# Optimization experiments

Hardware: AMD Instinct MI355X
Metric: run time of the kernel (lower is better)

Reference implementation:

```python
import jax, jax.numpy as jnp
import numpy as np

H = 12      # num_heads
EPS = 1e-5  # LayerNorm eps (torch default)


def _ln(x, g, b):
    m = x.mean(-1, keepdims=True)
    v = x.var(-1, keepdims=True)
    return (x - m) * jax.lax.rsqrt(v + EPS) * g + b


def _rot_half(x):
    x1, x2 = x[..., 0::2], x[..., 1::2]
    return jnp.stack((-x2, x1), axis=-1).reshape(x.shape)


def _rope_tables(n, head_dim):
    # rotary-embedding-torch: RotaryEmbedding(dim=head_dim//2, use_xpos=True),
    # theta=10000, scale_base=512. Only first rot=head_dim//2 dims are rotated.
    rot = head_dim // 2
    inv = 1.0 / (10000.0 ** (jnp.arange(0, rot, 2, dtype=jnp.float32) / rot))
    t = jnp.arange(n, dtype=jnp.float32)
    freqs = jnp.repeat(t[:, None] * inv[None, :], 2, axis=-1)  # (n, rot), interleaved
    base = (jnp.arange(0, rot, 2, dtype=jnp.float32) + 0.4 * rot) / (1.4 * rot)
    power = (t - n // 2) / 512.0
    sc = base[None, :] ** power[:, None]
    sc = jnp.concatenate([sc, sc], axis=-1)  # (n, rot), concatenated (library behavior)
    return jnp.cos(freqs), jnp.sin(freqs), sc


def _attn_path(xn, Wqkv, bqkv, Wproj, bproj, qg, qb, kg, kb, R, rg, rb):
    B, N, D = xn.shape
    d = D // H
    qkv = xn @ Wqkv + bqkv
    q, k, v = jnp.split(qkv, 3, axis=-1)
    hd = lambda t: t.reshape(B, N, H, d).transpose(0, 2, 1, 3)  # (B,H,N,d)
    q, k, v = hd(q), hd(k), hd(v)
    q = _ln(q, qg, qb)  # per-head QK LayerNorm
    k = _ln(k, kg, kb)
    cos, sin, sc = _rope_tables(N, d)
    rot = d // 2

    def rope(t, s):  # rotate only first rot dims
        tl, tr = t[..., :rot], t[..., rot:]
        tl = tl * cos * s + _rot_half(tl) * sin * s
        return jnp.concatenate([tl, tr], axis=-1)

    q = rope(q, sc)
    v = rope(v, 1.0 / sc)  # source applies rope to (q, v), not k

    scores = jnp.einsum('bhid,bhjd->bhij', q, k) / jnp.sqrt(jnp.asarray(d, xn.dtype))
    p = jax.nn.softmax(scores, axis=-1)
    # SDPA(q,k,ones_NN)[...,i,j] == sum_k p[...,i,k] for every j (constant over j).
    # All downstream ops (head-mix einsum, LayerNorm over heads, @ v) therefore
    # reduce exactly to the per-(b,i) computation below, avoiding an N^3 matmul.
    s = p.sum(-1)                              # (B,H,N)
    mix = jnp.einsum('bhi,hg->big', s, R)      # (B,N,H)
    w = _ln(mix, rg, rb)                       # reattn LayerNorm over head axis
    vsum = v.sum(axis=2)                       # (B,H,d); (w @ v) with w const over j
    y = jnp.einsum('big,bgd->bigd', w, vsum).reshape(B, N, D)
    return y @ Wproj + bproj


def _cgmlp(xn, W1, b1, gg, gb, cw, cb, W2, b2):
    h = jax.nn.gelu(xn @ W1 + b1, approximate=False)
    c2 = h.shape[-1] // 2
    xr, xg = h[..., :c2], h[..., c2:]
    xg = _ln(xg, gg, gb).transpose(0, 2, 1)  # (B,C,T)
    K = cw.shape[-1]
    xg = jax.lax.conv_general_dilated(xg, cw, (1,), [((K - 1) // 2, (K - 1) // 2)],
                                      dimension_numbers=('NCH', 'OIH', 'NCH'),
                                      feature_group_count=c2)  # depthwise conv1d
    xg = (xg + cb[None, :, None]).transpose(0, 2, 1)
    return (xr * xg) @ W2 + b2


def reference(x, Wqkv, bqkv, Wproj, bproj, qn_g, qn_b, kn_g, kn_b, reattn_w, rn_g, rn_b,
              ln1_g, ln1_b, ln2_g, ln2_b, ls1, ls2, W1, b1, gn_g, gn_b, conv_w, conv_b,
              W2, b2, Wout, bout):
    # eval mode: dropout / drop_path are identity
    xa = _ln(x, ln1_g, ln1_b)
    attn = sum(_attn_path(xa, Wqkv[p], bqkv[p], Wproj[p], bproj[p], qn_g[p], qn_b[p],
                          kn_g[p], kn_b[p], reattn_w[p], rn_g[p], rn_b[p])
               for p in range(2))
    x_attn = x + ls1 * attn
    xm = _ln(x, ln2_g, ln2_b)
    x_mlp = x + ls2 * _cgmlp(xm, W1, b1, gn_g, gn_b, conv_w, conv_b, W2, b2)
    xf = jnp.concatenate([x_attn, x_mlp], axis=-1)
    return xf @ Wout + bout + x


def setup_inputs():
    B, N, D, P = 4, 1024, 768, 2
    d = D // H
    C = 4 * D
    c2 = C // 2
    K = 21
    ks = iter(jax.random.split(jax.random.key(0), 16))
    nrm = lambda s, sd=0.02: jax.random.normal(next(ks), s, jnp.float32) * sd
    return {
        'x': jax.random.normal(next(ks), (B, N, D), jnp.float32),
        'Wqkv': nrm((P, D, 3 * D)), 'bqkv': jnp.zeros((P, 3 * D)),
        'Wproj': nrm((P, D, D)), 'bproj': jnp.zeros((P, D)),
        'qn_g': jnp.ones((P, d)), 'qn_b': jnp.zeros((P, d)),
        'kn_g': jnp.ones((P, d)), 'kn_b': jnp.zeros((P, d)),
        'reattn_w': jax.random.normal(next(ks), (P, H, H), jnp.float32),
        'rn_g': jnp.ones((P, H)), 'rn_b': jnp.zeros((P, H)),
        'ln1_g': jnp.ones((D,)), 'ln1_b': jnp.zeros((D,)),
        'ln2_g': jnp.ones((D,)), 'ln2_b': jnp.zeros((D,)),
        'ls1': jnp.full((D,), 0.01, jnp.float32), 'ls2': jnp.full((D,), 0.01, jnp.float32),
        'W1': nrm((D, C)), 'b1': jnp.zeros((C,)),
        'gn_g': jnp.ones((c2,)), 'gn_b': jnp.zeros((c2,)),
        'conv_w': nrm((c2, 1, K), 0.1), 'conv_b': jnp.zeros((c2,)),
        'W2': nrm((c2, D)), 'b2': jnp.zeros((D,)),
        'Wout': nrm((2 * D, D)), 'bout': jnp.zeros((D,)),
    }
```

## Files before the change

### kernel.cpp

```cpp
#include <hip/hip_runtime.h>
#include <hip/hip_bf16.h>

typedef short s16x8 __attribute__((ext_vector_type(8)));
typedef float f32x4 __attribute__((ext_vector_type(4)));

#define C2 1536

__device__ __forceinline__ float b2f(ushort u){ return __uint_as_float(((unsigned)u)<<16); }
__device__ __forceinline__ ushort f2b(float f){ unsigned u = __float_as_uint(f); return (ushort)((u + 0x7fffu + ((u>>16)&1u)) >> 16); }

template<int EPI, int BM, int BN>
__global__ __launch_bounds__(256) void gemm_bf16(
    const ushort* __restrict__ A, const ushort* __restrict__ BT,
    int M, int N, int K,
    const float* __restrict__ bias, const float* __restrict__ scale,
    const float* __restrict__ xres,
    ushort* __restrict__ o16, ushort* __restrict__ o16b, float* __restrict__ o32)
{
    constexpr int CA = BM*4, CB = BN*4;
    constexpr int WM = BM/2, WN = BN/2;
    constexpr int MT = WM/16, NT = WN/16;
    __shared__ ushort Al[BM*32];
    __shared__ ushort Bl[BN*32];
    const int t = threadIdx.x;
    const int m0 = blockIdx.y*BM, n0 = blockIdx.x*BN;
    const int lane = t & 63, wv = t >> 6;
    const int wm = (wv>>1)*WM, wn = (wv&1)*WN;
    const int r0 = lane & 15, q = lane >> 4;

    const int cA0 = t, cA1 = t + 256;
    const int cB0 = t, cB1 = t + 256;
    const int rA0 = ((cA0>>6)<<4)|(cA0&15), kA0 = ((cA0>>4)&3)<<3;
    const int rA1 = ((cA1>>6)<<4)|(cA1&15), kA1 = ((cA1>>4)&3)<<3;
    const int rB0 = ((cB0>>6)<<4)|(cB0&15), kB0 = ((cB0>>4)&3)<<3;
    const int rB1 = ((cB1>>6)<<4)|(cB1&15), kB1 = ((cB1>>4)&3)<<3;
    const ushort* gA0 = A  + (size_t)(m0+rA0)*K + kA0;
    const ushort* gB0 = BT + (size_t)(n0+rB0)*K + kB0;
    const ushort* gA1 = A  + (size_t)(m0+(CA>256?rA1:0))*K + kA1;
    const ushort* gB1 = BT + (size_t)(n0+(CB>256?rB1:0))*K + kB1;

    f32x4 acc[MT][NT];
    #pragma unroll
    for (int i=0;i<MT;++i)
        #pragma unroll
        for (int j=0;j<NT;++j) acc[i][j] = (f32x4){0.f,0.f,0.f,0.f};

    const int nkt = K >> 5;
    uint4 ra0, rb0, ra1, rb1;
    ra0 = *(const uint4*)gA0;
    rb0 = *(const uint4*)gB0;
    if constexpr (CA > 256) ra1 = *(const uint4*)gA1;
    if constexpr (CB > 256) rb1 = *(const uint4*)gB1;

    for (int kt = 0; kt < nkt; ++kt) {
        __syncthreads();
        *(uint4*)&Al[cA0*8] = ra0;
        *(uint4*)&Bl[cB0*8] = rb0;
        if constexpr (CA > 256) *(uint4*)&Al[cA1*8] = ra1;
        if constexpr (CB > 256) *(uint4*)&Bl[cB1*8] = rb1;
        __syncthreads();
        if (kt+1 < nkt) {
            ra0 = *(const uint4*)(gA0 + (kt+1)*32);
            rb0 = *(const uint4*)(gB0 + (kt+1)*32);
            if constexpr (CA > 256) ra1 = *(const uint4*)(gA1 + (kt+1)*32);
            if constexpr (CB > 256) rb1 = *(const uint4*)(gB1 + (kt+1)*32);
        }
        s16x8 af[MT], bfr[NT];
        #pragma unroll
        for (int mt=0; mt<MT; ++mt) af[mt]  = *(const s16x8*)&Al[(((wm>>4)+mt)*64 + lane)*8];
        #pragma unroll
        for (int nt=0; nt<NT; ++nt) bfr[nt] = *(const s16x8*)&Bl[(((wn>>4)+nt)*64 + lane)*8];
        #pragma unroll
        for (int mt=0; mt<MT; ++mt)
            #pragma unroll
            for (int nt=0; nt<NT; ++nt)
                acc[mt][nt] = __builtin_amdgcn_mfma_f32_16x16x32_bf16(af[mt], bfr[nt], acc[mt][nt], 0,0,0);
    }

    #pragma unroll
    for (int mt=0; mt<MT; ++mt) {
        #pragma unroll
        for (int nt=0; nt<NT; ++nt) {
            int col = n0 + wn + nt*16 + r0;
            #pragma unroll
            for (int r=0; r<4; ++r) {
                int row = m0 + wm + mt*16 + q*4 + r;
                float v = acc[mt][nt][r];
                if (EPI == 0) {
                    o16[(size_t)row*N + col] = f2b(v + bias[col]);
                } else if (EPI == 1) {
                    v += bias[col];
                    float g = 0.5f*v*(1.0f + erff(v*0.70710678118f));
                    if (col < C2) o16 [(size_t)row*C2 + col]        = f2b(g);
                    else          o16b[(size_t)row*C2 + (col - C2)] = f2b(g);
                } else if (EPI == 2) {
                    v += bias[col];
                    o16[(size_t)row*1536 + 768 + col] = f2b(xres[(size_t)row*768 + col] + scale[col]*v);
                } else {
                    o32[(size_t)row*768 + col] = v + bias[col] + xres[(size_t)row*768 + col];
                }
            }
        }
    }
}

__global__ __launch_bounds__(256) void pack_bt(const float* __restrict__ src, ushort* __restrict__ dst,
                                               int K, int ld, int coff)
{
    __shared__ float tl[32*33];
    int kt = blockIdx.x*32, nt = blockIdx.y*32;
    int nl = threadIdx.x & 31, kg = threadIdx.x >> 5;
    #pragma unroll
    for (int kk=0; kk<4; ++kk) {
        int k = kg*4 + kk;
        tl[k*33 + nl] = src[(size_t)(kt + k)*ld + coff + nt + nl];
    }
    __syncthreads();
    int kcol = threadIdx.x & 31, ng = threadIdx.x >> 5;
    #pragma unroll
    for (int nn=0; nn<4; ++nn) {
        int nrow = ng*4 + nn;
        dst[(size_t)(nt + nrow)*K + kt + kcol] = f2b(tl[kcol*33 + nrow]);
    }
}

__global__ __launch_bounds__(256) void pack_bv(const float* __restrict__ bqkv, float* __restrict__ bvp)
{
    int idx = blockIdx.x*256 + threadIdx.x;
    if (idx < 1536) bvp[idx] = bqkv[(idx/768)*2304 + 1536 + (idx%768)];
}

__global__ __launch_bounds__(256) void ln_x_kernel(const float* __restrict__ x,
    const float* __restrict__ g1, const float* __restrict__ b1,
    const float* __restrict__ g2, const float* __restrict__ b2,
    ushort* __restrict__ xa, ushort* __restrict__ xm)
{
    __shared__ float sb[8];
    int row = blockIdx.x; int t = threadIdx.x;
    float v[3]; float s = 0.f, ss = 0.f;
    #pragma unroll
    for (int e=0; e<3; ++e) { v[e] = x[(size_t)row*768 + t + e*256]; s += v[e]; ss += v[e]*v[e]; }
    for (int o=32; o>0; o>>=1){ s += __shfl_down(s,o,64); ss += __shfl_down(ss,o,64); }
    int lane = t&63, w = t>>6;
    if (lane==0){ sb[w]=s; sb[4+w]=ss; }
    __syncthreads();
    s = sb[0]+sb[1]+sb[2]+sb[3]; ss = sb[4]+sb[5]+sb[6]+sb[7];
    float mean = s*(1.f/768.f);
    float var  = ss*(1.f/768.f) - mean*mean;
    float rstd = rsqrtf(var + 1e-5f);
    #pragma unroll
    for (int e=0; e<3; ++e){
        int c = t + e*256;
        float n = (v[e]-mean)*rstd;
        xa[(size_t)row*768 + c] = f2b(n*g1[c] + b1[c]);
        xm[(size_t)row*768 + c] = f2b(n*g2[c] + b2[c]);
    }
}

__global__ __launch_bounds__(256) void prep_kernel(
    float* __restrict__ w1t, float* __restrict__ w2t, float* __restrict__ wvec,
    float* __restrict__ attn_c, float* __restrict__ vsum,
    const float* __restrict__ R, const float* __restrict__ rng,
    const float* __restrict__ rnb, const float* __restrict__ bproj)
{
    int idx = blockIdx.x*256 + threadIdx.x;
    {
        int i = idx >> 6, j = idx & 63;
        float w1, w2;
        if (j < 32) {
            int m = j >> 1;
            float inv = powf(10000.f, -(float)m*(1.f/16.f));
            float fr = (float)i * inv;
            float c = cosf(fr), sn = sinf(fr);
            float power = ((float)i - 512.f) * (1.f/512.f);
            float basev = (2.f*(float)(j & 15) + 12.8f) * (1.f/44.8f);
            float sfac = powf(basev, -power);
            w1 = c * sfac;
            w2 = ((j & 1) ? sn : -sn) * sfac;
        } else { w1 = 1.f; w2 = 0.f; }
        w1t[idx] = w1; w2t[idx] = w2;
    }
    if (blockIdx.x >= 1 && blockIdx.x <= 12) {
        int k = (blockIdx.x-1)*256 + threadIdx.x;
        int o = k % 768;
        attn_c[k] = bproj[o] + bproj[768 + o];
    }
    if (blockIdx.x >= 13 && blockIdx.x <= 36) {
        int k = (blockIdx.x-13)*256 + threadIdx.x;
        vsum[k] = 0.f;
    }
    if (blockIdx.x == 0) {
        __shared__ float mixs[24];
        __shared__ float ws[24];
        int t = threadIdx.x;
        if (t < 24) {
            int p = t / 12, g = t % 12;
            float m = 0.f;
            for (int h=0; h<12; ++h) m += R[p*144 + h*12 + g];
            mixs[t] = m;
        }
        __syncthreads();
        if (t < 2) {
            float mean=0.f, var=0.f;
            for (int g=0; g<12; ++g) mean += mixs[t*12+g];
            mean *= (1.f/12.f);
            for (int g=0; g<12; ++g){ float d = mixs[t*12+g]-mean; var += d*d; }
            var *= (1.f/12.f);
            float rstd = rsqrtf(var + 1e-5f);
            for (int g=0; g<12; ++g)
                ws[t*12+g] = (mixs[t*12+g]-mean)*rstd*rng[t*12+g] + rnb[t*12+g];
        }
        __syncthreads();
        if (t < 24) wvec[t] = ws[t];
    }
}

__global__ __launch_bounds__(256) void rope_reduce(const ushort* __restrict__ V,
    const float* __restrict__ w1t, const float* __restrict__ w2t, float* __restrict__ vsum)
{
    int col = blockIdx.x*256 + threadIdx.x;
    int b = blockIdx.y;
    int i0 = blockIdx.z * 256;
    int j = col & 63;
    float acc = 0.f;
    const ushort* vp = V + (size_t)(b*1024 + i0)*1536;
    #pragma unroll 4
    for (int i=0; i<256; ++i) {
        float v1 = b2f(vp[(size_t)i*1536 + col]);
        float v2 = b2f(vp[(size_t)i*1536 + (col^1)]);
        int ii = i0 + i;
        acc += w1t[ii*64 + j]*v1 + w2t[ii*64 + j]*v2;
    }
    atomicAdd(&vsum[b*1536 + col], acc);
}

__global__ __launch_bounds__(256) void attn_gemm(const float* __restrict__ vsum,
    const float* __restrict__ wvec, const float* __restrict__ Wproj, float* __restrict__ attn_c)
{
    int o  = blockIdx.x*256 + threadIdx.x;
    int c0 = blockIdx.y * 96;
    int b  = blockIdx.z;
    int p  = c0 / 768;
    float acc = 0.f;
    #pragma unroll 4
    for (int cc=0; cc<96; ++cc) {
        int c = c0 + cc;
        int cl = c - p*768;
        float y = wvec[p*12 + (cl>>6)] * vsum[b*1536 + c];
        acc += y * Wproj[(size_t)p*589824 + (size_t)cl*768 + o];
    }
    atomicAdd(&attn_c[b*768 + o], acc);
}

__global__ __launch_bounds__(256) void xf_left(const float* __restrict__ x, const float* __restrict__ ls1,
    const float* __restrict__ attn_c, ushort* __restrict__ xf)
{
    int col = blockIdx.x*256 + threadIdx.x;
    int row = blockIdx.y;
    xf[(size_t)row*1536 + col] = f2b(x[(size_t)row*768 + col] + ls1[col]*attn_c[(row>>10)*768 + col]);
}

__global__ __launch_bounds__(256) void ln_gate(const ushort* __restrict__ xg,
    const float* __restrict__ g, const float* __restrict__ bta, ushort* __restrict__ out)
{
    __shared__ float sb[8];
    int row = blockIdx.x, t = threadIdx.x;
    float v[6]; float s=0.f, ss=0.f;
    #pragma unroll
    for (int e=0;e<6;++e){ v[e] = b2f(xg[(size_t)row*1536 + t + e*256]); s+=v[e]; ss+=v[e]*v[e]; }
    for (int o=32; o>0; o>>=1){ s += __shfl_down(s,o,64); ss += __shfl_down(ss,o,64); }
    int lane = t&63, w = t>>6;
    if (lane==0){ sb[w]=s; sb[4+w]=ss; }
    __syncthreads();
    s = sb[0]+sb[1]+sb[2]+sb[3]; ss = sb[4]+sb[5]+sb[6]+sb[7];
    float mean = s*(1.f/1536.f);
    float var  = ss*(1.f/1536.f) - mean*mean;
    float rstd = rsqrtf(var + 1e-5f);
    #pragma unroll
    for (int e=0;e<6;++e){
        int c = t + e*256;
        out[(size_t)row*1536 + c] = f2b((v[e]-mean)*rstd*g[c] + bta[c]);
    }
}

#define CROWS 128
#define CIN   (CROWS + 20)
#define CSTR  72
__global__ __launch_bounds__(256) void conv_mul(const ushort* __restrict__ xgln,
    const float* __restrict__ cw, const float* __restrict__ cb,
    const ushort* __restrict__ xr, ushort* __restrict__ u)
{
    __shared__ ushort tile[CIN * CSTR];
    const int c0 = blockIdx.x * 64;
    const int i0 = blockIdx.y * CROWS;
    const int b  = blockIdx.z;
    const int t  = threadIdx.x;
    const size_t base = (size_t)b*1024*1536;

    #pragma unroll
    for (int it = 0; it < 5; ++it) {
        int idx = it*256 + t;
        if (idx < CIN*8) {
            int r  = idx >> 3;
            int cq = (idx & 7) * 8;
            int si = i0 + r - 10;
            uint4 val = make_uint4(0u,0u,0u,0u);
            if (si >= 0 && si < 1024)
                val = *(const uint4*)(xgln + base + (size_t)si*1536 + c0 + cq);
            *(uint4*)&tile[r*CSTR + cq] = val;
        }
    }
    __syncthreads();

    const int ch = t & 63;
    const int o0 = (t >> 6) * 32;
    const int c  = c0 + ch;

    float w[21];
    #pragma unroll
    for (int k=0; k<21; ++k) w[k] = cw[c*21 + k];
    const float bias = cb[c];

    float win[21];
    #pragma unroll
    for (int j=0; j<20; ++j) win[j] = b2f(tile[(o0+j)*CSTR + ch]);

    #pragma unroll
    for (int j=0; j<32; ++j) {
        win[(j+20)%21] = b2f(tile[(o0+j+20)*CSTR + ch]);
        float acc = bias;
        #pragma unroll
        for (int k=0; k<21; ++k) acc += win[(j+k)%21] * w[k];
        size_t off = base + (size_t)(i0+o0+j)*1536 + c;
        u[off] = f2b(b2f(xr[off]) * acc);
    }
}

extern "C" void kernel_launch(void* const* d_in, const int* in_sizes, int n_in,
                              void* d_out, int out_size, void* d_ws, size_t ws_size,
                              hipStream_t stream)
{
    const float* x     = (const float*)d_in[0];
    const float* Wqkv  = (const float*)d_in[1];
    const float* bqkv  = (const float*)d_in[2];
    const float* Wproj = (const float*)d_in[3];
    const float* bproj = (const float*)d_in[4];
    const float* Rw    = (const float*)d_in[9];
    const float* rng   = (const float*)d_in[10];
    const float* rnb   = (const float*)d_in[11];
    const float* ln1g  = (const float*)d_in[12];
    const float* ln1b  = (const float*)d_in[13];
    const float* ln2g  = (const float*)d_in[14];
    const float* ln2b  = (const float*)d_in[15];
    const float* ls1   = (const float*)d_in[16];
    const float* ls2   = (const float*)d_in[17];
    const float* W1    = (const float*)d_in[18];
    const float* b1    = (const float*)d_in[19];
    const float* gng   = (const float*)d_in[20];
    const float* gnb   = (const float*)d_in[21];
    const float* cw    = (const float*)d_in[22];
    const float* cb    = (const float*)d_in[23];
    const float* W2    = (const float*)d_in[24];
    const float* b2    = (const float*)d_in[25];
    const float* Wout  = (const float*)d_in[26];
    const float* bout  = (const float*)d_in[27];
    float* out = (float*)d_out;

    char* ws = (char*)d_ws;
    size_t off = 0;
    auto alloc = [&](size_t bytes)->char* {
        char* p = ws + off;
        off += (bytes + 255) & ~(size_t)255;
        return p;
    };
    ushort* WvT   = (ushort*)alloc(1536*768*2);
    ushort* W1T   = (ushort*)alloc(3072*768*2);
    ushort* W2T   = (ushort*)alloc(768*1536*2);
    ushort* WoutT = (ushort*)alloc(768*1536*2);
    float*  bvp   = (float*)alloc(1536*4);
    float*  w1t   = (float*)alloc(65536*4);
    float*  w2t   = (float*)alloc(65536*4);
    float*  wvec  = (float*)alloc(24*4);
    float*  attnc = (float*)alloc(3072*4);
    float*  vsum  = (float*)alloc(6144*4);
    ushort* xa16  = (ushort*)alloc(4096*768*2);
    ushort* xm16  = (ushort*)alloc(4096*768*2);
    ushort* V16   = (ushort*)alloc(4096*1536*2);
    ushort* xg16  = (ushort*)alloc(4096*1536*2);
    ushort* xf16  = (ushort*)alloc(4096*1536*2);
    ushort* xgln  = xa16;
    ushort* xr16  = V16;
    ushort* u16   = xg16;
    (void)ws_size; (void)n_in; (void)in_sizes; (void)out_size;

    for (int p = 0; p < 2; ++p)
        pack_bt<<<dim3(24, 24), 256, 0, stream>>>(Wqkv + (size_t)p*768*2304, WvT + (size_t)p*768*768,
                                                  768, 2304, 1536);
    pack_bt<<<dim3(24, 96), 256, 0, stream>>>(W1,   W1T,   768,  3072, 0);
    pack_bt<<<dim3(48, 24), 256, 0, stream>>>(W2,   W2T,   1536, 768,  0);
    pack_bt<<<dim3(48, 24), 256, 0, stream>>>(Wout, WoutT, 1536, 768,  0);
    pack_bv<<<dim3(6), 256, 0, stream>>>(bqkv, bvp);
    prep_kernel<<<dim3(256), 256, 0, stream>>>(w1t, w2t, wvec, attnc, vsum, Rw, rng, rnb, bproj);

    ln_x_kernel<<<dim3(4096), 256, 0, stream>>>(x, ln1g, ln1b, ln2g, ln2b, xa16, xm16);

    gemm_bf16<0,64,128><<<dim3(12, 64), 256, 0, stream>>>(xa16, WvT, 4096, 1536, 768,
                                                   bvp, nullptr, nullptr, V16, nullptr, nullptr);
    rope_reduce<<<dim3(6, 4, 4), 256, 0, stream>>>(V16, w1t, w2t, vsum);
    attn_gemm<<<dim3(3, 16, 4), 256, 0, stream>>>(vsum, wvec, Wproj, attnc);
    xf_left<<<dim3(3, 4096), 256, 0, stream>>>(x, ls1, attnc, xf16);

    gemm_bf16<1,128,128><<<dim3(24, 32), 256, 0, stream>>>(xm16, W1T, 4096, 3072, 768,
                                                   b1, nullptr, nullptr, xr16, xg16, nullptr);
    ln_gate<<<dim3(4096), 256, 0, stream>>>(xg16, gng, gnb, xgln);
    conv_mul<<<dim3(24, 8, 4), 256, 0, stream>>>(xgln, cw, cb, xr16, u16);
    gemm_bf16<2,64,64><<<dim3(12, 64), 256, 0, stream>>>(u16, W2T, 4096, 768, 1536,
                                                  b2, ls2, x, xf16, nullptr, nullptr);
    gemm_bf16<3,64,64><<<dim3(12, 64), 256, 0, stream>>>(xf16, WoutT, 4096, 768, 1536,
                                                  bout, nullptr, x, nullptr, nullptr, out);
}
```

Measured before the change: 385.2 us.

## Fold W2 into Wout and reassociate V rope-reduction to skip V GEMM

The code precomputes a combined weight (ls2-scaled Wout lower half times W2, plus the summed Wout halves) so the W2 GEMM and the Wout GEMM merge into one K=2304 GEMM over [x | u]. Constant terms (attention output, biases) are folded into a per-batch bias vector cvec. The full 4096x1536 V projection GEMM plus rope reduction becomes a small transpose, GEMMs of xa^T against the rope tables, and a contraction with WvT, so the large V intermediate is never built. This cuts FLOPs and memory traffic but adds several small serial kernels and extra weight prep per call. It also changes rounding, since x is rounded to bf16 and the W2·Wout product is precomputed in bf16.

```diff
diff --git a/kernel.cpp b/kernel.cpp
--- a/kernel.cpp
+++ b/kernel.cpp
@@ -12,9 +12,8 @@
 template<int EPI, int BM, int BN>
 __global__ __launch_bounds__(256) void gemm_bf16(
     const ushort* __restrict__ A, const ushort* __restrict__ BT,
-    int M, int N, int K,
-    const float* __restrict__ bias, const float* __restrict__ scale,
-    const float* __restrict__ xres,
+    int M, int N, int K, int lda,
+    const float* __restrict__ bias, const float* __restrict__ xres,
     ushort* __restrict__ o16, ushort* __restrict__ o16b, float* __restrict__ o32)
 {
     constexpr int CA = BM*4, CB = BN*4;
@@ -29,15 +28,12 @@
     const int r0 = lane & 15, q = lane >> 4;
 
     const int cA0 = t, cA1 = t + 256;
-    const int cB0 = t, cB1 = t + 256;
     const int rA0 = ((cA0>>6)<<4)|(cA0&15), kA0 = ((cA0>>4)&3)<<3;
     const int rA1 = ((cA1>>6)<<4)|(cA1&15), kA1 = ((cA1>>4)&3)<<3;
-    const int rB0 = ((cB0>>6)<<4)|(cB0&15), kB0 = ((cB0>>4)&3)<<3;
-    const int rB1 = ((cB1>>6)<<4)|(cB1&15), kB1 = ((cB1>>4)&3)<<3;
-    const ushort* gA0 = A  + (size_t)(m0+rA0)*K + kA0;
-    const ushort* gB0 = BT + (size_t)(n0+rB0)*K + kB0;
-    const ushort* gA1 = A  + (size_t)(m0+(CA>256?rA1:0))*K + kA1;
-    const ushort* gB1 = BT + (size_t)(n0+(CB>256?rB1:0))*K + kB1;
+    const ushort* gA0 = A  + (size_t)(m0+rA0)*lda + kA0;
+    const ushort* gB0 = BT + (size_t)(n0+rA0)*K   + kA0;
+    const ushort* gA1 = A  + (size_t)(m0+(CA>256?rA1:0))*lda + kA1;
+    const ushort* gB1 = BT + (size_t)(n0+(CB>256?rA1:0))*K   + kA1;
 
     f32x4 acc[MT][NT];
     #pragma unroll
@@ -55,9 +51,9 @@
     for (int kt = 0; kt < nkt; ++kt) {
         __syncthreads();
         *(uint4*)&Al[cA0*8] = ra0;
-        *(uint4*)&Bl[cB0*8] = rb0;
+        *(uint4*)&Bl[cA0*8] = rb0;
         if constexpr (CA > 256) *(uint4*)&Al[cA1*8] = ra1;
-        if constexpr (CB > 256) *(uint4*)&Bl[cB1*8] = rb1;
+        if constexpr (CB > 256) *(uint4*)&Bl[cA1*8] = rb1;
         __syncthreads();
         if (kt+1 < nkt) {
             ra0 = *(const uint4*)(gA0 + (kt+1)*32);
@@ -86,18 +82,17 @@
             for (int r=0; r<4; ++r) {
                 int row = m0 + wm + mt*16 + q*4 + r;
                 float v = acc[mt][nt][r];
-                if (EPI == 0) {
-                    o16[(size_t)row*N + col] = f2b(v + bias[col]);
-                } else if (EPI == 1) {
+                if (EPI == 1) {
                     v += bias[col];
                     float g = 0.5f*v*(1.0f + erff(v*0.70710678118f));
                     if (col < C2) o16 [(size_t)row*C2 + col]        = f2b(g);
                     else          o16b[(size_t)row*C2 + (col - C2)] = f2b(g);
-                } else if (EPI == 2) {
-                    v += bias[col];
-                    o16[(size_t)row*1536 + 768 + col] = f2b(xres[(size_t)row*768 + col] + scale[col]*v);
-                } else {
-                    o32[(size_t)row*768 + col] = v + bias[col] + xres[(size_t)row*768 + col];
+                } else if (EPI == 3) {
+                    o32[(size_t)row*768 + col] = v + bias[(row>>10)*768 + col] + xres[(size_t)row*768 + col];
+                } else if (EPI == 4) {
+                    o16[(size_t)row*2304 + 768 + col] = f2b(v);
+                } else if (EPI == 5) {
+                    o32[(size_t)row*N + col] = v;
                 }
             }
         }
@@ -105,7 +100,7 @@
 }
 
 __global__ __launch_bounds__(256) void pack_bt(const float* __restrict__ src, ushort* __restrict__ dst,
-                                               int K, int ld, int coff)
+                                               int K, int ld, int coff, const float* __restrict__ scale)
 {
     __shared__ float tl[32*33];
     int kt = blockIdx.x*32, nt = blockIdx.y*32;
@@ -120,8 +115,53 @@
     #pragma unroll
     for (int nn=0; nn<4; ++nn) {
         int nrow = ng*4 + nn;
-        dst[(size_t)(nt + nrow)*K + kt + kcol] = f2b(tl[kcol*33 + nrow]);
-    }
+        float s = scale ? scale[kt + kcol] : 1.0f;
+        dst[(size_t)(nt + nrow)*K + kt + kcol] = f2b(tl[kcol*33 + nrow] * s);
+    }
+}
+
+__global__ __launch_bounds__(256) void pack_wsum(const float* __restrict__ Wout, ushort* __restrict__ dst)
+{
+    __shared__ float tl[32*33];
+    int kt = blockIdx.x*32, nt = blockIdx.y*32;
+    int nl = threadIdx.x & 31, kg = threadIdx.x >> 5;
+    #pragma unroll
+    for (int kk=0; kk<4; ++kk) {
+        int k = kg*4 + kk;
+        tl[k*33 + nl] = Wout[(size_t)(kt + k)*768 + nt + nl] + Wout[(size_t)(768 + kt + k)*768 + nt + nl];
+    }
+    __syncthreads();
+    int kcol = threadIdx.x & 31, ng = threadIdx.x >> 5;
+    #pragma unroll
+    for (int nn=0; nn<4; ++nn) {
+        int nrow = ng*4 + nn;
+        dst[(size_t)(nt + nrow)*2304 + kt + kcol] = f2b(tl[kcol*33 + nrow]);
+    }
+}
+
+__global__ __launch_bounds__(256) void tr_bf16(const ushort* __restrict__ src, ushort* __restrict__ dst)
+{
+    __shared__ ushort tl[32*33];
+    int rt = blockIdx.x*32, ct = blockIdx.y*32;
+    int cl = threadIdx.x & 31, rg = threadIdx.x >> 5;
+    #pragma unroll
+    for (int rr=0; rr<4; ++rr) {
+        int r = rg*4 + rr;
+        tl[r*33 + cl] = src[(size_t)(rt + r)*768 + ct + cl];
+    }
+    __syncthreads();
+    int rcol = threadIdx.x & 31, cg = threadIdx.x >> 5;
+    #pragma unroll
+    for (int cc=0; cc<4; ++cc) {
+        int crow = cg*4 + cc;
+        dst[(size_t)(ct + crow)*4096 + rt + rcol] = tl[rcol*33 + crow];
+    }
+}
+
+__global__ __launch_bounds__(256) void pack_cast(const float* __restrict__ src, ushort* __restrict__ dst)
+{
+    int idx = blockIdx.x*256 + threadIdx.x;
+    dst[idx] = f2b(src[idx]);
 }
 
 __global__ __launch_bounds__(256) void pack_bv(const float* __restrict__ bqkv, float* __restrict__ bvp)
@@ -133,7 +173,7 @@
 __global__ __launch_bounds__(256) void ln_x_kernel(const float* __restrict__ x,
     const float* __restrict__ g1, const float* __restrict__ b1,
     const float* __restrict__ g2, const float* __restrict__ b2,
-    ushort* __restrict__ xa, ushort* __restrict__ xm)
+    ushort* __restrict__ xa, ushort* __restrict__ xm, ushort* __restrict__ xb)
 {
     __shared__ float sb[8];
     int row = blockIdx.x; int t = threadIdx.x;
@@ -154,14 +194,15 @@
         float n = (v[e]-mean)*rstd;
         xa[(size_t)row*768 + c] = f2b(n*g1[c] + b1[c]);
         xm[(size_t)row*768 + c] = f2b(n*g2[c] + b2[c]);
+        xb[(size_t)row*2304 + c] = f2b(v[e]);
     }
 }
 
 __global__ __launch_bounds__(256) void prep_kernel(
-    float* __restrict__ w1t, float* __restrict__ w2t, float* __restrict__ wvec,
-    float* __restrict__ attn_c, float* __restrict__ vsum,
+    float* __restrict__ w1t, float* __restrict__ w2t, ushort* __restrict__ w12T,
+    float* __restrict__ wvec, float* __restrict__ attn_c, float* __restrict__ cvec,
     const float* __restrict__ R, const float* __restrict__ rng,
-    const float* __restrict__ rnb, const float* __restrict__ bproj)
+    const float* __restrict__ rnb, const float* __restrict__ bproj, const float* __restrict__ bout)
 {
     int idx = blockIdx.x*256 + threadIdx.x;
     {
@@ -179,15 +220,17 @@
             w2 = ((j & 1) ? sn : -sn) * sfac;
         } else { w1 = 1.f; w2 = 0.f; }
         w1t[idx] = w1; w2t[idx] = w2;
+        w12T[(size_t)j*1024 + i]        = f2b(w1);
+        w12T[(size_t)(64+j)*1024 + i]   = f2b(w2);
     }
     if (blockIdx.x >= 1 && blockIdx.x <= 12) {
         int k = (blockIdx.x-1)*256 + threadIdx.x;
         int o = k % 768;
         attn_c[k] = bproj[o] + bproj[768 + o];
     }
-    if (blockIdx.x >= 13 && blockIdx.x <= 36) {
+    if (blockIdx.x >= 13 && blockIdx.x <= 24) {
         int k = (blockIdx.x-13)*256 + threadIdx.x;
-        vsum[k] = 0.f;
+        cvec[k] = bout[k % 768];
     }
     if (blockIdx.x == 0) {
         __shared__ float mixs[24];
@@ -215,23 +258,40 @@
     }
 }
 
-__global__ __launch_bounds__(256) void rope_reduce(const ushort* __restrict__ V,
-    const float* __restrict__ w1t, const float* __restrict__ w2t, float* __restrict__ vsum)
-{
-    int col = blockIdx.x*256 + threadIdx.x;
+__global__ __launch_bounds__(256) void s12_kernel(const float* __restrict__ w1t,
+    const float* __restrict__ w2t, float* __restrict__ S12)
+{
+    int t = threadIdx.x;
+    if (t < 128) {
+        const float* w = (t < 64) ? w1t : w2t;
+        int j = t & 63;
+        float s = 0.f;
+        for (int i = 0; i < 1024; ++i) s += w[i*64 + j];
+        S12[t] = s;
+    }
+}
+
+__global__ __launch_bounds__(256) void vsum_assemble(const float* __restrict__ T12,
+    const ushort* __restrict__ WvT, const float* __restrict__ bvp, const float* __restrict__ S12,
+    float* __restrict__ vsum)
+{
+    int c = blockIdx.x*256 + threadIdx.x;
     int b = blockIdx.y;
-    int i0 = blockIdx.z * 256;
-    int j = col & 63;
-    float acc = 0.f;
-    const ushort* vp = V + (size_t)(b*1024 + i0)*1536;
-    #pragma unroll 4
-    for (int i=0; i<256; ++i) {
-        float v1 = b2f(vp[(size_t)i*1536 + col]);
-        float v2 = b2f(vp[(size_t)i*1536 + (col^1)]);
-        int ii = i0 + i;
-        acc += w1t[ii*64 + j]*v1 + w2t[ii*64 + j]*v2;
-    }
-    atomicAdd(&vsum[b*1536 + col], acc);
+    int j = c & 63;
+    float acc = bvp[c]*S12[j] + bvp[c^1]*S12[64+j];
+    const ushort* wr1 = WvT + (size_t)c*768;
+    const ushort* wr2 = WvT + (size_t)(c^1)*768;
+    const float* Tb = T12 + (size_t)b*768*128;
+    for (int k0 = 0; k0 < 768; k0 += 8) {
+        s16x8 v1 = *(const s16x8*)(wr1 + k0);
+        s16x8 v2 = *(const s16x8*)(wr2 + k0);
+        #pragma unroll
+        for (int e=0; e<8; ++e) {
+            acc += Tb[(size_t)(k0+e)*128 + j]      * b2f((ushort)v1[e]);
+            acc += Tb[(size_t)(k0+e)*128 + 64 + j] * b2f((ushort)v2[e]);
+        }
+    }
+    vsum[b*1536 + c] = acc;
 }
 
 __global__ __launch_bounds__(256) void attn_gemm(const float* __restrict__ vsum,
@@ -252,12 +312,21 @@
     atomicAdd(&attn_c[b*768 + o], acc);
 }
 
-__global__ __launch_bounds__(256) void xf_left(const float* __restrict__ x, const float* __restrict__ ls1,
-    const float* __restrict__ attn_c, ushort* __restrict__ xf)
-{
-    int col = blockIdx.x*256 + threadIdx.x;
-    int row = blockIdx.y;
-    xf[(size_t)row*1536 + col] = f2b(x[(size_t)row*768 + col] + ls1[col]*attn_c[(row>>10)*768 + col]);
+__global__ __launch_bounds__(256) void cvec_kernel(const float* __restrict__ attn_c,
+    const float* __restrict__ ls1, const float* __restrict__ ls2, const float* __restrict__ b2,
+    const float* __restrict__ Wout, float* __restrict__ cvec)
+{
+    int o  = blockIdx.x*256 + threadIdx.x;
+    int c0 = blockIdx.y * 96;
+    int b  = blockIdx.z;
+    float acc = 0.f;
+    #pragma unroll 4
+    for (int cc=0; cc<96; ++cc) {
+        int c = c0 + cc;
+        float w = (c < 768) ? (ls1[c]*attn_c[b*768 + c]) : (ls2[c-768]*b2[c-768]);
+        acc += w * Wout[(size_t)c*768 + o];
+    }
+    atomicAdd(&cvec[b*768 + o], acc);
 }
 
 __global__ __launch_bounds__(256) void ln_gate(const ushort* __restrict__ xg,
@@ -331,8 +400,9 @@
         float acc = bias;
         #pragma unroll
         for (int k=0; k<21; ++k) acc += win[(j+k)%21] * w[k];
-        size_t off = base + (size_t)(i0+o0+j)*1536 + c;
-        u[off] = f2b(b2f(xr[off]) * acc);
+        int ri = b*1024 + i0 + o0 + j;
+        float xrv = b2f(xr[(size_t)ri*1536 + c]);
+        u[(size_t)ri*2304 + 768 + c] = f2b(xrv * acc);
     }
 }
 
@@ -375,47 +445,58 @@
     };
     ushort* WvT   = (ushort*)alloc(1536*768*2);
     ushort* W1T   = (ushort*)alloc(3072*768*2);
-    ushort* W2T   = (ushort*)alloc(768*1536*2);
-    ushort* WoutT = (ushort*)alloc(768*1536*2);
+    ushort* W2bf  = (ushort*)alloc(1536*768*2);
+    ushort* atW   = (ushort*)alloc(768*768*2);
+    ushort* BTbig = (ushort*)alloc(768*2304*2);
     float*  bvp   = (float*)alloc(1536*4);
     float*  w1t   = (float*)alloc(65536*4);
     float*  w2t   = (float*)alloc(65536*4);
+    ushort* w12T  = (ushort*)alloc(128*1024*2);
+    float*  S12   = (float*)alloc(128*4);
     float*  wvec  = (float*)alloc(24*4);
     float*  attnc = (float*)alloc(3072*4);
     float*  vsum  = (float*)alloc(6144*4);
+    float*  cvec  = (float*)alloc(3072*4);
     ushort* xa16  = (ushort*)alloc(4096*768*2);
     ushort* xm16  = (ushort*)alloc(4096*768*2);
-    ushort* V16   = (ushort*)alloc(4096*1536*2);
+    ushort* xr16  = (ushort*)alloc(4096*1536*2);
     ushort* xg16  = (ushort*)alloc(4096*1536*2);
-    ushort* xf16  = (ushort*)alloc(4096*1536*2);
+    ushort* Abig  = (ushort*)alloc(4096*2304*2);
+    float*  T12   = (float*)W2bf;
+    ushort* xaT   = xg16;
     ushort* xgln  = xa16;
-    ushort* xr16  = V16;
-    ushort* u16   = xg16;
     (void)ws_size; (void)n_in; (void)in_sizes; (void)out_size;
 
     for (int p = 0; p < 2; ++p)
         pack_bt<<<dim3(24, 24), 256, 0, stream>>>(Wqkv + (size_t)p*768*2304, WvT + (size_t)p*768*768,
-                                                  768, 2304, 1536);
-    pack_bt<<<dim3(24, 96), 256, 0, stream>>>(W1,   W1T,   768,  3072, 0);
-    pack_bt<<<dim3(48, 24), 256, 0, stream>>>(W2,   W2T,   1536, 768,  0);
-    pack_bt<<<dim3(48, 24), 256, 0, stream>>>(Wout, WoutT, 1536, 768,  0);
+                                                  768, 2304, 1536, nullptr);
+    pack_bt<<<dim3(24, 96), 256, 0, stream>>>(W1, W1T, 768, 3072, 0, nullptr);
+    pack_cast<<<dim3(4608), 256, 0, stream>>>(W2, W2bf);
+    pack_bt<<<dim3(24, 24), 256, 0, stream>>>(Wout + 768*768, atW, 768, 768, 0, ls2);
+    pack_wsum<<<dim3(24, 24), 256, 0, stream>>>(Wout, BTbig);
+    gemm_bf16<4,64,128><<<dim3(12, 12), 256, 0, stream>>>(atW, W2bf, 768, 1536, 768, 768,
+                                                  nullptr, nullptr, BTbig, nullptr, nullptr);
     pack_bv<<<dim3(6), 256, 0, stream>>>(bqkv, bvp);
-    prep_kernel<<<dim3(256), 256, 0, stream>>>(w1t, w2t, wvec, attnc, vsum, Rw, rng, rnb, bproj);
-
-    ln_x_kernel<<<dim3(4096), 256, 0, stream>>>(x, ln1g, ln1b, ln2g, ln2b, xa16, xm16);
-
-    gemm_bf16<0,64,128><<<dim3(12, 64), 256, 0, stream>>>(xa16, WvT, 4096, 1536, 768,
-                                                   bvp, nullptr, nullptr, V16, nullptr, nullptr);
-    rope_reduce<<<dim3(6, 4, 4), 256, 0, stream>>>(V16, w1t, w2t, vsum);
+    prep_kernel<<<dim3(256), 256, 0, stream>>>(w1t, w2t, w12T, wvec, attnc, cvec,
+                                               Rw, rng, rnb, bproj, bout);
+    s12_kernel<<<dim3(1), 256, 0, stream>>>(w1t, w2t, S12);
+
+    ln_x_kernel<<<dim3(4096), 256, 0, stream>>>(x, ln1g, ln1b, ln2g, ln2b, xa16, xm16, Abig);
+
+    tr_bf16<<<dim3(128, 24), 256, 0, stream>>>(xa16, xaT);
+    for (int b = 0; b < 4; ++b)
+        gemm_bf16<5,64,64><<<dim3(2, 12), 256, 0, stream>>>(xaT + b*1024, w12T, 768, 128, 1024, 4096,
+                                                  nullptr, nullptr, nullptr, nullptr,
+                                                  T12 + (size_t)b*768*128);
+    vsum_assemble<<<dim3(6, 4), 256, 0, stream>>>(T12, WvT, bvp, S12, vsum);
     attn_gemm<<<dim3(3, 16, 4), 256, 0, stream>>>(vsum, wvec, Wproj, attnc);
-    xf_left<<<dim3(3, 4096), 256, 0, stream>>>(x, ls1, attnc, xf16);
-
-    gemm_bf16<1,128,128><<<dim3(24, 32), 256, 0, stream>>>(xm16, W1T, 4096, 3072, 768,
-                                                   b1, nullptr, nullptr, xr16, xg16, nullptr);
+    cvec_kernel<<<dim3(3, 16, 4), 256, 0, stream>>>(attnc, ls1, ls2, b2, Wout, cvec);
+
+    gemm_bf16<1,128,128><<<dim3(24, 32), 256, 0, stream>>>(xm16, W1T, 4096, 3072, 768, 768,
+                                                  b1, nullptr, xr16, xg16, nullptr);
     ln_gate<<<dim3(4096), 256, 0, stream>>>(xg16, gng, gnb, xgln);
-    conv_mul<<<dim3(24, 8, 4), 256, 0, stream>>>(xgln, cw, cb, xr16, u16);
-    gemm_bf16<2,64,64><<<dim3(12, 64), 256, 0, stream>>>(u16, W2T, 4096, 768, 1536,
-                                                  b2, ls2, x, xf16, nullptr, nullptr);
-    gemm_bf16<3,64,64><<<dim3(12, 64), 256, 0, stream>>>(xf16, WoutT, 4096, 768, 1536,
-                                                  bout, nullptr, x, nullptr, nullptr, out);
-}
+    conv_mul<<<dim3(24, 8, 4), 256, 0, stream>>>(xgln, cw, cb, xr16, Abig);
+
+    gemm_bf16<3,64,64><<<dim3(12, 64), 256, 0, stream>>>(Abig, BTbig, 4096, 768, 2304, 2304,
+                                                  cvec, x, nullptr, nullptr, out);
+}
```

Result: slower. 470.1 us (+22.0%).
